# Optimization experiments

Hardware: AMD Instinct MI355X
Metric: run time of the kernel (lower is better)

Reference implementation:

```python
import jax, jax.numpy as jnp
import numpy as np

PRECS = 1e-6
# [min, max] scaling ranges for the 12 XAJ parameters (order matches parameters[:, i, :])
PARA_SCALE = [[0.3, 2.0], [0.0, 5.0], [0.01, 100.0], [0.01, 100.0], [0.01, 200.0],
              [0.09, 1.0], [0.01, 100.0], [0.0, 10.0], [0.01, 0.7], [0.01, 0.7],
              [0.0, 0.998], [0.0, 0.998]]


def setup_inputs() -> dict:
    key = jax.random.key(0)
    k1, k2 = jax.random.split(key)
    Nstep, Ngrid, mu = 365, 2000, 8
    # col 0 = P (mm/d), col 2 = PET (mm/d); col 1 unused by the model
    x = jax.random.uniform(k1, (Nstep, Ngrid, 3), dtype=jnp.float32) * 10.0
    parameters = jax.random.uniform(k2, (Ngrid, 12, mu), dtype=jnp.float32)
    return {"x": x, "parameters": parameters, "mu": mu}


def _xaj(x, parameters, mu):
    P = x[:, :, 0]          # [T, Ngrid]
    PET = x[:, :, 2]        # [T, Ngrid]  (index 2, matching the original code)
    Ngrid = x.shape[1]

    sc = lambda a, i: PARA_SCALE[i][0] + a * (PARA_SCALE[i][1] - PARA_SCALE[i][0])
    (parKE, parB, parWUM, parWLM, parWM, parC, parSM, parEX,
     parKI_, parKG_, parCI, parCG) = [sc(parameters[:, i, :], i) for i in range(12)]

    wdm = jnp.maximum(parWM - parWUM - parWLM, 0.0)
    sum_k = parKI_ + parKG_
    parKI = jnp.where(sum_k < 1.0, parKI_, (1.0 - PRECS) * parKI_ / (sum_k + PRECS))
    parKG = jnp.where(sum_k < 1.0, parKG_, (1.0 - PRECS) * parKG_ / (sum_k + PRECS))

    init_state = jnp.full((Ngrid, mu), 0.001, dtype=jnp.float32)
    WU0 = WL0 = WD0 = S0 = QI0 = QG0 = FR0_init = init_state

    def step(carry, inp):
        WU, WL, WD, S, FR0, QI, QG = carry
        P_row, PET_row = inp                      # each [Ngrid]
        P_t = P_row[:, None]                      # broadcast over mu
        PET_t = PET_row[:, None] * parKE

        # three-layer evapotranspiration
        EU = jnp.minimum(PET_t, WU + P_t)
        D = jnp.maximum(PET_t - EU, 0.0)
        wet_excess = jnp.maximum(WL - parC * parWLM, 0.0)
        wet_ratio = wet_excess / (wet_excess + 1.0)
        EL_wet = D * WL / (parWLM + PRECS)
        EL_dry = jnp.minimum(parC * D, WL)
        EL = jnp.maximum(wet_ratio * EL_wet + (1.0 - wet_ratio) * EL_dry, 0.0)
        EL = jnp.minimum(EL, WL)
        D_res = jnp.maximum(D - EL, 0.0)
        ED = jnp.minimum(parC * D_res, WD)
        E = EU + EL + ED

        # saturation-excess runoff
        PE = jnp.maximum(P_t - E, 0.0)
        W = WU + WL + WD
        WMM = parWM * (1.0 + parB)
        base_W = jnp.maximum(1.0 - W / (parWM + PRECS), PRECS)
        A = WMM * (1.0 - base_W ** (1.0 / (1.0 + parB)))
        ratio = jnp.minimum((PE + A) / (WMM + PRECS), 1.0)
        R_per = jnp.where(PE + A < WMM,
                          PE - (parWM - W) + parWM * (1.0 - ratio) ** (1.0 + parB),
                          PE - (parWM - W))
        R_per = jnp.maximum(R_per, 0.0)

        # soil moisture update (fill top-down, deplete top-down)
        dW = P_t - E - R_per
        dpos = jnp.maximum(dW, 0.0)
        fill_u = jnp.minimum(dpos, jnp.maximum(parWUM - WU, 0.0))
        WU = WU + fill_u; dpos = dpos - fill_u
        fill_l = jnp.minimum(dpos, jnp.maximum(parWLM - WL, 0.0))
        WL = WL + fill_l; dpos = dpos - fill_l
        fill_d = jnp.minimum(dpos, jnp.maximum(wdm - WD, 0.0))
        WD = WD + fill_d
        dneg = jnp.maximum(-dW, 0.0)
        sub_u = jnp.minimum(dneg, WU)
        WU = WU - sub_u; dneg = dneg - sub_u
        sub_l = jnp.minimum(dneg, WL)
        WL = WL - sub_l; dneg = dneg - sub_l
        sub_d = jnp.minimum(dneg, WD)
        WD = WD - sub_d

        # free-water reservoir + three-flow separation
        FR_new = R_per / (PE + PRECS)
        FR = jnp.where(PE > 0.0, FR_new, FR0)
        FR = jnp.clip(FR, 0.0, 1.0)
        S_eq = jnp.minimum(S * FR0 / (FR + PRECS), parSM)
        SMM = parSM * (1.0 + parEX)
        ratio_s = jnp.maximum(1.0 - S_eq / (parSM + PRECS), PRECS)
        AU = SMM * (1.0 - ratio_s ** (1.0 / (1.0 + parEX)))
        ratio_pa = jnp.minimum((PE + AU) / (SMM + PRECS), 1.0)
        RS1 = (PE + S_eq - parSM + parSM * (1.0 - ratio_pa) ** (1.0 + parEX)) * FR
        RS2 = (PE + S_eq - parSM) * FR
        RS = jnp.where(PE + AU < SMM, RS1, RS2)
        RS = jnp.minimum(jnp.maximum(RS, 0.0), R_per)
        S = jnp.minimum(S_eq + (R_per - RS) / (FR + PRECS), parSM)
        RI = parKI * S * FR
        RG = parKG * S * FR
        S = S * (1.0 - parKI - parKG)

        # linear reservoirs
        QI = parCI * QI + (1.0 - parCI) * RI
        QG = parCG * QG + (1.0 - parCG) * RG

        return (WU, WL, WD, S, FR, QI, QG), (RS, QI, QG, E)

    carry0 = (WU0, WL0, WD0, S0, FR0_init, QI0, QG0)
    _, (QS_inflow, QI_inflow, QG_inflow, ET_series) = jax.lax.scan(step, carry0, (P, PET))

    QSave = QS_inflow.mean(-1, keepdims=True)
    QIave = QI_inflow.mean(-1, keepdims=True)
    QGave = QG_inflow.mean(-1, keepdims=True)
    ETave = ET_series.mean(-1, keepdims=True)
    river_inflow = QS_inflow + QI_inflow + QG_inflow
    Qs = river_inflow.mean(-1, keepdims=True)   # muwts is None
    # [Nstep, Ngrid, 5]
    return jnp.concatenate([Qs, QSave, QIave, QGave, ETave], axis=-1)


def reference(x, parameters, mu):
    return _xaj(x, parameters, mu)
```

## Files before the change

kernel.cpp:

```cpp
#include <hip/hip_runtime.h>

#define PRECS 1e-6f

__device__ __forceinline__ float fpow(float b, float e) {
    return __builtin_amdgcn_exp2f(e * __builtin_amdgcn_logf(b));
}

__device__ __forceinline__ float frcp(float v) {
    return __builtin_amdgcn_rcpf(v);
}

template <int CTRL>
__device__ __forceinline__ float dpp_mov(float v) {
    return __int_as_float(
        __builtin_amdgcn_update_dpp(0, __float_as_int(v), CTRL, 0xF, 0xF, true));
}

__device__ __forceinline__ float rsum8(float v) {
    v += dpp_mov<0xB1>(v);
    v += dpp_mov<0x4E>(v);
    v += dpp_mov<0x141>(v);
    return v;
}

__global__ __launch_bounds__(192, 1) void xaj_kernel(
    const float* __restrict__ x,
    const float* __restrict__ prm,
    float* __restrict__ out)
{
    constexpr int Nstep = 365, Ngrid = 2000;
    constexpr int xstride = Ngrid * 3;
    constexpr int K = 8;
    constexpr int NBLK = 46;

    const int wid  = (int)threadIdx.x >> 6;
    const int lane = (int)threadIdx.x & 63;
    const int g = blockIdx.x * 8 + (lane >> 3);
    const int m = lane & 7;

    __shared__ float4 stA[2][K][64];
    __shared__ float4 stB[2][K][64];

    const float lo[12] = {0.3f,0.0f,0.01f,0.01f,0.01f,0.09f,0.01f,0.0f,0.01f,0.01f,0.0f,0.0f};
    const float hi[12] = {2.0f,5.0f,100.0f,100.0f,200.0f,1.0f,100.0f,10.0f,0.7f,0.7f,0.998f,0.998f};
    float p[12];
    const float* pb = prm + (size_t)g * 96 + m;
#pragma unroll
    for (int i = 0; i < 12; ++i)
        p[i] = lo[i] + pb[i * 8] * (hi[i] - lo[i]);

    const float KE=p[0], B=p[1], WUM=p[2], WLM=p[3], WM=p[4], C=p[5],
                SM=p[6], EX=p[7], KI_=p[8], KG_=p[9], CI=p[10], CG=p[11];

    const float wdm  = fmaxf(WM - WUM - WLM, 0.f);
    const float sumk = KI_ + KG_;
    const float nrm  = (1.f - PRECS) / (sumk + PRECS);
    const float KI   = (sumk < 1.f) ? KI_ : KI_ * nrm;
    const float KG   = (sumk < 1.f) ? KG_ : KG_ * nrm;
    const float expB = 1.f + B,  invB  = 1.f / expB;
    const float WMM  = WM * expB;
    const float expEX= 1.f + EX, invEX = 1.f / expEX;
    const float SMM  = SM * expEX;
    const float inv_WLM = 1.f / (WLM + PRECS);
    const float inv_WM  = 1.f / (WM  + PRECS);
    const float inv_WMM = 1.f / (WMM + PRECS);
    const float inv_SM  = 1.f / (SM  + PRECS);
    const float inv_SMM = 1.f / (SMM + PRECS);
    const float oneK = 1.f - KI - KG;
    const float omCI = 1.f - CI, omCG = 1.f - CG;
    const float CWLM = C * WLM;
    const float inv1p = 1.f / (1.f + PRECS);
    const float eps2  = fmaxf(PRECS, fmaf(-SM, inv_SM, 1.f));

    float WU = 0.001f, WL = 0.001f, WD = 0.001f;
    float S = 0.001f, FR0 = 0.001f, QI = 0.001f, QG = 0.001f;
    float iFR0 = frcp(FR0 + PRECS);
    const float wa = (m == 0 || m == 1) ? 0.125f : 0.f;
    const float wb = (m == 0 || m == 2) ? 0.125f : 0.f;
    const float wc = (m == 0 || m == 3) ? 0.125f : 0.f;
    const float wd = (m >= 4) ? 0.125f : 0.f;
    const int   col = (m < 4) ? m : 4;
    float* outp = out + (size_t)g * 5 + col;
    const size_t ostr = (size_t)Ngrid * 5;

    const float* xg = x + (size_t)g * 3;
    float PA[K], EA[K], PB_[K], EB_[K];

    auto ISSUE = [&](float* Pr, float* Er, int blk) {
#pragma unroll
        for (int k = 0; k < K; ++k) {
            int t = blk * K + k;
            t = (t < Nstep) ? t : Nstep - 1;
            const float* xq = xg + (size_t)t * xstride;
            Pr[k] = xq[0];
            Er[k] = xq[2];
        }
    };

    auto PRODUCE = [&](const float* Pr, const float* Er, float4* sa) {
#pragma unroll
        for (int k = 0; k < K; ++k) {
            const float Pt = Pr[k], PETr = Er[k];
            const float PET_t = PETr * KE;
            const float EU = fminf(PET_t, WU + Pt);
            const float D  = fmaxf(PET_t - Pt - WU, 0.f);
            const float we = fmaxf(WL - CWLM, 0.f);
            const float wr = we * frcp(we + 1.f);
            const float cwet = wr * WL * inv_WLM;
            const float ELdry = fminf(C * D, WL);
            const float EL = fminf(fmaxf(fmaf(1.f - wr, ELdry, cwet * D), 0.f), WL);
            const float ED = fminf(C * fmaxf(D - EL, 0.f), WD);
            const float E  = EU + EL + ED;
            const float PE = fmaxf(Pt - E, 0.f);
            const float W = WU + WL + WD;
            const float base_W = fmaxf(fmaf(-W, inv_WM, 1.f), PRECS);
            const float pw1 = fpow(base_W, invB);
            const float omr = fmaxf(fmaf(-PE, inv_WMM, pw1), 0.f);
            const float R_per = fmaxf(fmaf(WM, fpow(omr, expB), PE + (W - WM)), 0.f);
            const float dW = Pt - E - R_per;
            const float capD = fmaxf(wdm, WD);
            const float cum0 = WU + dW;
            const float WUn  = __builtin_amdgcn_fmed3f(cum0, 0.f, WUM);
            const float cum1 = WL + (cum0 - WUn);
            const float WLn  = __builtin_amdgcn_fmed3f(cum1, 0.f, WLM);
            const float cum2 = WD + (cum1 - WLn);
            const float WDn  = __builtin_amdgcn_fmed3f(cum2, 0.f, capD);
            WU = WUn; WL = WLn; WD = WDn;
            sa[k * 64 + lane] = make_float4(PE, R_per, E, 0.f);
        }
    };

    auto BSTEP = [&](const float4* sa, float4* sb) {
        float4 ra[K];
#pragma unroll
        for (int k = 0; k < K; ++k)
            ra[k] = sa[k * 64 + lane];
        float FRn[K], iFRn[K];
#pragma unroll
        for (int k = 0; k < K; ++k) {
            const float q  = frcp(ra[k].x + PRECS);
            const float aa = ra[k].y * q;
            FRn[k]  = fminf(aa, 1.f);
            iFRn[k] = fmaxf(frcp(aa + PRECS), inv1p);
        }
#pragma unroll
        for (int k = 0; k < K; ++k) {
            const float PE = ra[k].x, R_per = ra[k].y;
            const bool wet = PE > 0.f;
            const float FR  = wet ? FRn[k]  : FR0;
            const float iFR = wet ? iFRn[k] : iFR0;
            const float sf  = S * FR0;
            const float sf2 = sf * inv_SM;
            const float S_eq = fminf(sf * iFR, SM);
            const float ratio_s = fmaxf(fmaf(-sf2, iFR, 1.f), eps2);
            const float u   = fpow(ratio_s, invEX);
            const float om2 = fmaxf(fmaf(-PE, inv_SMM, u), 0.f);
            const float base = (PE - SM) + S_eq;
            float RS = fmaf(SM, fpow(om2, expEX), base) * FR;
            RS = __builtin_amdgcn_fmed3f(RS, 0.f, R_per);
            const float Sn = fminf(fmaf(R_per - RS, iFR, S_eq), SM);
            const float RI = (KI * FR) * Sn;
            const float RG = (KG * FR) * Sn;
            S  = Sn * oneK;
            QI = fmaf(omCI, RI, CI * QI);
            QG = fmaf(omCG, RG, CG * QG);
            FR0 = FR; iFR0 = iFR;
            sb[k * 64 + lane] = make_float4(RS, QI, QG, ra[k].z);
        }
    };

    auto CSTEP = [&](const float4* sb, int blk) {
        float4 rb[K];
#pragma unroll
        for (int k = 0; k < K; ++k)
            rb[k] = sb[k * 64 + lane];
        const int t0 = blk * K;
#pragma unroll
        for (int k = 0; k < K; ++k) {
            const float u0 = rsum8(rb[k].x);
            const float u1 = rsum8(rb[k].y);
            const float u2 = rsum8(rb[k].z);
            const float u3 = rsum8(rb[k].w);
            const float v = fmaf(u0, wa, fmaf(u1, wb, fmaf(u2, wc, u3 * wd)));
            if (t0 + k < Nstep)
                outp[(size_t)(t0 + k) * ostr] = v;
        }
    };

    if (wid == 0) ISSUE(PA, EA, 0);

#pragma unroll 1
    for (int it = 0; it < 24; ++it) {
        const int p0 = 2 * it, p1 = 2 * it + 1;
        if (wid == 0) {
            if (p0 < NBLK) {
                ISSUE(PB_, EB_, (p0 + 1 < NBLK) ? p0 + 1 : NBLK - 1);
                PRODUCE(PA, EA, &stA[0][0][0]);
            }
        } else if (wid == 1) {
            if (p0 >= 2 && p0 <= NBLK)
                BSTEP(&stA[1][0][0], &stB[1][0][0]);
        } else {
            if (p0 >= 2)
                CSTEP(&stB[0][0][0], p0 - 2);
        }
        __syncthreads();
        if (wid == 0) {
            if (p1 < NBLK) {
                ISSUE(PA, EA, (p1 + 1 < NBLK) ? p1 + 1 : NBLK - 1);
                PRODUCE(PB_, EB_, &stA[1][0][0]);
            }
        } else if (wid == 1) {
            if (p1 <= NBLK)
                BSTEP(&stA[0][0][0], &stB[0][0][0]);
        } else {
            if (p1 >= 3)
                CSTEP(&stB[1][0][0], p1 - 2);
        }
        __syncthreads();
    }
}

extern "C" void kernel_launch(void* const* d_in, const int* in_sizes, int n_in,
                              void* d_out, int out_size, void* d_ws, size_t ws_size,
                              hipStream_t stream) {
    const float* x   = (const float*)d_in[0];
    const float* prm = (const float*)d_in[1];
    float* out = (float*)d_out;
    xaj_kernel<<<250, 192, 0, stream>>>(x, prm, out);
}
```

Before: 59.37 us.

## Rebalance warp pipeline: move input loads and QI/QG recurrence to third wave

The chunk size is doubled (K=16, half as many blocks), which halves the number of barrier rounds. Global loads of P and PET move from the first-stage wave to the output wave, which prefetches them and hands them over through a new LDS buffer with PET already scaled by KE. The linear-reservoir QI/QG recurrence also moves from the second stage into the reduction wave, shortening the serial critical path of the two recurrent stages. The cost is more LDS and register use per wave, plus a longer pipeline fill relative to the block count.

Measured after the change: 58.07 us. 2.2% less time.

```diff
diff --git a/kernel.cpp b/kernel.cpp
--- a/kernel.cpp
+++ b/kernel.cpp
@@ -30,14 +30,15 @@
 {
     constexpr int Nstep = 365, Ngrid = 2000;
     constexpr int xstride = Ngrid * 3;
-    constexpr int K = 8;
-    constexpr int NBLK = 46;
+    constexpr int K = 16;
+    constexpr int NBLK = 23;
 
     const int wid  = (int)threadIdx.x >> 6;
     const int lane = (int)threadIdx.x & 63;
     const int g = blockIdx.x * 8 + (lane >> 3);
     const int m = lane & 7;
 
+    __shared__ float2 stIn[2][K][64];
     __shared__ float4 stA[2][K][64];
     __shared__ float4 stB[2][K][64];
 
@@ -73,8 +74,10 @@
     const float eps2  = fmaxf(PRECS, fmaf(-SM, inv_SM, 1.f));
 
     float WU = 0.001f, WL = 0.001f, WD = 0.001f;
-    float S = 0.001f, FR0 = 0.001f, QI = 0.001f, QG = 0.001f;
+    float S = 0.001f, FR0 = 0.001f;
     float iFR0 = frcp(FR0 + PRECS);
+    float QI = 0.001f, QG = 0.001f;
+    const float cKI = omCI * KI, cKG = omCG * KG;
     const float wa = (m == 0 || m == 1) ? 0.125f : 0.f;
     const float wb = (m == 0 || m == 2) ? 0.125f : 0.f;
     const float wc = (m == 0 || m == 3) ? 0.125f : 0.f;
@@ -82,26 +85,17 @@
     const int   col = (m < 4) ? m : 4;
     float* outp = out + (size_t)g * 5 + col;
     const size_t ostr = (size_t)Ngrid * 5;
-
     const float* xg = x + (size_t)g * 3;
-    float PA[K], EA[K], PB_[K], EB_[K];
-
-    auto ISSUE = [&](float* Pr, float* Er, int blk) {
-#pragma unroll
-        for (int k = 0; k < K; ++k) {
-            int t = blk * K + k;
-            t = (t < Nstep) ? t : Nstep - 1;
-            const float* xq = xg + (size_t)t * xstride;
-            Pr[k] = xq[0];
-            Er[k] = xq[2];
-        }
-    };
-
-    auto PRODUCE = [&](const float* Pr, const float* Er, float4* sa) {
-#pragma unroll
-        for (int k = 0; k < K; ++k) {
-            const float Pt = Pr[k], PETr = Er[k];
-            const float PET_t = PETr * KE;
+    float Pr[K], Er[K];
+
+    auto ASTEP = [&](int buf) {
+        float2 rin[K];
+#pragma unroll
+        for (int k = 0; k < K; ++k)
+            rin[k] = stIn[buf][k][lane];
+#pragma unroll
+        for (int k = 0; k < K; ++k) {
+            const float Pt = rin[k].x, PET_t = rin[k].y;
             const float EU = fminf(PET_t, WU + Pt);
             const float D  = fmaxf(PET_t - Pt - WU, 0.f);
             const float we = fmaxf(WL - CWLM, 0.f);
@@ -126,15 +120,15 @@
             const float cum2 = WD + (cum1 - WLn);
             const float WDn  = __builtin_amdgcn_fmed3f(cum2, 0.f, capD);
             WU = WUn; WL = WLn; WD = WDn;
-            sa[k * 64 + lane] = make_float4(PE, R_per, E, 0.f);
-        }
-    };
-
-    auto BSTEP = [&](const float4* sa, float4* sb) {
+            stA[buf][k][lane] = make_float4(PE, R_per, E, 0.f);
+        }
+    };
+
+    auto BSTEP = [&](int buf) {
         float4 ra[K];
 #pragma unroll
         for (int k = 0; k < K; ++k)
-            ra[k] = sa[k * 64 + lane];
+            ra[k] = stA[buf][k][lane];
         float FRn[K], iFRn[K];
 #pragma unroll
         for (int k = 0; k < K; ++k) {
@@ -159,63 +153,73 @@
             float RS = fmaf(SM, fpow(om2, expEX), base) * FR;
             RS = __builtin_amdgcn_fmed3f(RS, 0.f, R_per);
             const float Sn = fminf(fmaf(R_per - RS, iFR, S_eq), SM);
-            const float RI = (KI * FR) * Sn;
-            const float RG = (KG * FR) * Sn;
             S  = Sn * oneK;
-            QI = fmaf(omCI, RI, CI * QI);
-            QG = fmaf(omCG, RG, CG * QG);
             FR0 = FR; iFR0 = iFR;
-            sb[k * 64 + lane] = make_float4(RS, QI, QG, ra[k].z);
-        }
-    };
-
-    auto CSTEP = [&](const float4* sb, int blk) {
+            stB[buf][k][lane] = make_float4(RS, FR * Sn, ra[k].z, 0.f);
+        }
+    };
+
+    auto CISSUE = [&](int blk) {
+#pragma unroll
+        for (int k = 0; k < K; ++k) {
+            int t = blk * K + k;
+            t = (t < Nstep) ? t : Nstep - 1;
+            const float* xq = xg + (size_t)t * xstride;
+            Pr[k] = xq[0];
+            Er[k] = xq[2];
+        }
+    };
+    auto CWRITE = [&](int buf) {
+#pragma unroll
+        for (int k = 0; k < K; ++k)
+            stIn[buf][k][lane] = make_float2(Pr[k], Er[k] * KE);
+    };
+    auto CRED = [&](int buf, int q) {
         float4 rb[K];
 #pragma unroll
         for (int k = 0; k < K; ++k)
-            rb[k] = sb[k * 64 + lane];
-        const int t0 = blk * K;
-#pragma unroll
-        for (int k = 0; k < K; ++k) {
+            rb[k] = stB[buf][k][lane];
+        const int t0 = q * K;
+#pragma unroll
+        for (int k = 0; k < K; ++k) {
+            QI = fmaf(CI, QI, cKI * rb[k].y);
+            QG = fmaf(CG, QG, cKG * rb[k].y);
             const float u0 = rsum8(rb[k].x);
-            const float u1 = rsum8(rb[k].y);
-            const float u2 = rsum8(rb[k].z);
-            const float u3 = rsum8(rb[k].w);
+            const float u1 = rsum8(QI);
+            const float u2 = rsum8(QG);
+            const float u3 = rsum8(rb[k].z);
             const float v = fmaf(u0, wa, fmaf(u1, wb, fmaf(u2, wc, u3 * wd)));
             if (t0 + k < Nstep)
                 outp[(size_t)(t0 + k) * ostr] = v;
         }
     };
 
-    if (wid == 0) ISSUE(PA, EA, 0);
+    if (wid == 2) { CISSUE(0); CWRITE(0); }
+    __syncthreads();
 
 #pragma unroll 1
-    for (int it = 0; it < 24; ++it) {
-        const int p0 = 2 * it, p1 = 2 * it + 1;
+    for (int i = 0; i < 13; ++i) {
+        const int p0 = 2 * i, p1 = 2 * i + 1;
         if (wid == 0) {
-            if (p0 < NBLK) {
-                ISSUE(PB_, EB_, (p0 + 1 < NBLK) ? p0 + 1 : NBLK - 1);
-                PRODUCE(PA, EA, &stA[0][0][0]);
-            }
+            if (p0 < NBLK) ASTEP(0);
         } else if (wid == 1) {
-            if (p0 >= 2 && p0 <= NBLK)
-                BSTEP(&stA[1][0][0], &stB[1][0][0]);
+            if (p0 >= 1 && p0 <= NBLK) BSTEP(1);
         } else {
-            if (p0 >= 2)
-                CSTEP(&stB[0][0][0], p0 - 2);
+            const bool ld = (p0 + 1 < NBLK);
+            if (ld) CISSUE(p0 + 1);
+            if (p0 >= 2) CRED(0, p0 - 2);
+            if (ld) CWRITE(1);
         }
         __syncthreads();
         if (wid == 0) {
-            if (p1 < NBLK) {
-                ISSUE(PA, EA, (p1 + 1 < NBLK) ? p1 + 1 : NBLK - 1);
-                PRODUCE(PB_, EB_, &stA[1][0][0]);
-            }
+            if (p1 < NBLK) ASTEP(1);
         } else if (wid == 1) {
-            if (p1 <= NBLK)
-                BSTEP(&stA[0][0][0], &stB[0][0][0]);
+            if (p1 <= NBLK) BSTEP(0);
         } else {
-            if (p1 >= 3)
-                CSTEP(&stB[1][0][0], p1 - 2);
+            const bool ld = (p1 + 1 < NBLK);
+            if (ld) CISSUE(p1 + 1);
+            if (p1 >= 2) CRED(1, p1 - 2);
+            if (ld) CWRITE(0);
         }
         __syncthreads();
     }
```
